# Kernel optimization log

Measured on AMD Instinct MI355X. Metric: run time of the kernel, lower is better.

## Reference

```python
import jax, jax.numpy as jnp
import numpy as np

B, S, E = 8, 2048, 1024

def setup_inputs() -> dict:
    key = jax.random.key(0)
    ks = jax.random.split(key, 7)
    scale = 1.0 / np.sqrt(E)
    return {
        "x": jax.random.normal(ks[0], (B, S, E), dtype=jnp.float32),
        "Wq": jax.random.normal(ks[1], (E, E), dtype=jnp.float32) * scale,
        "bq": jax.random.normal(ks[2], (E,), dtype=jnp.float32) * 0.01,
        "Wk": jax.random.normal(ks[3], (E, E), dtype=jnp.float32) * scale,
        "bk": jax.random.normal(ks[4], (E,), dtype=jnp.float32) * 0.01,
        "Wv": jax.random.normal(ks[5], (E, E), dtype=jnp.float32) * scale,
        "bv": jax.random.normal(ks[6], (E,), dtype=jnp.float32) * 0.01,
    }

def reference(x, Wq, bq, Wk, bk, Wv, bv):
    # torch Linear: y = x @ W^T + b
    q = jnp.einsum('bse,fe->bsf', x, Wq) + bq  # [B,S,E]
    k = jnp.einsum('bse,fe->bsf', x, Wk) + bk
    v = jnp.einsum('bse,fe->bsf', x, Wv) + bv
    # unscaled, unmasked single-head attention (faithful to source)
    scores = jnp.einsum('bqe,bke->bqk', q, k)  # [B,S,S]
    attn = jax.nn.softmax(scores, axis=-1)
    return jnp.einsum('bqk,bke->bqe', attn, v)  # [B,S,E]
```

## Files before the change

### kernel.cpp

```cpp
#include <hip/hip_runtime.h>
#include <math.h>

typedef _Float16 f16;
typedef _Float16 f16x8 __attribute__((ext_vector_type(8)));
typedef _Float16 f16x4 __attribute__((ext_vector_type(4)));
typedef float f32x4v __attribute__((ext_vector_type(4)));

#define Bb 8
#define Ss 2048
#define Ee 1024
#define BSr (Bb*Ss)

__device__ __forceinline__ void gll16(const void* gp, void* lp) {
    __builtin_amdgcn_global_load_lds(
        (const __attribute__((address_space(1))) unsigned int*)gp,
        (__attribute__((address_space(3))) unsigned int*)lp,
        16, 0, 0);
}

#define MFMA16(a, b, c) __builtin_amdgcn_mfma_f32_16x16x32_f16((a), (b), (c), 0, 0, 0)
#define SBAR() asm volatile("s_barrier" ::: "memory")

__global__ __launch_bounds__(256)
void split_weights(const float* __restrict__ Wq, const float* __restrict__ Wk,
                   const float* __restrict__ Wv,
                   f16* __restrict__ Wqh, f16* __restrict__ Wql,
                   f16* __restrict__ Wkh, f16* __restrict__ Wkl,
                   f16* __restrict__ Wvh)
{
    const int i = (blockIdx.x * 256 + threadIdx.x) * 4;
    float4 q = *(const float4*)&Wq[i];
    float4 k = *(const float4*)&Wk[i];
    float4 v = *(const float4*)&Wv[i];
    f16x4 qh4, ql4, kh4, kl4, vh4;
#define SPL(val, h4, l4, idx) { f16 hh = (f16)(val); h4[idx] = hh; l4[idx] = (f16)((val) - (float)hh); }
    SPL(q.x, qh4, ql4, 0) SPL(q.y, qh4, ql4, 1) SPL(q.z, qh4, ql4, 2) SPL(q.w, qh4, ql4, 3)
    SPL(k.x, kh4, kl4, 0) SPL(k.y, kh4, kl4, 1) SPL(k.z, kh4, kl4, 2) SPL(k.w, kh4, kl4, 3)
#undef SPL
    vh4[0] = (f16)v.x; vh4[1] = (f16)v.y; vh4[2] = (f16)v.z; vh4[3] = (f16)v.w;
    *(f16x4*)&Wqh[i] = qh4; *(f16x4*)&Wql[i] = ql4;
    *(f16x4*)&Wkh[i] = kh4; *(f16x4*)&Wkl[i] = kl4;
    *(f16x4*)&Wvh[i] = vh4;
}

__global__ __launch_bounds__(256)
void split_x(const float* __restrict__ x, f16* __restrict__ xh)
{
    const int i = (blockIdx.x * 256 + threadIdx.x) * 4;
    float4 v = *(const float4*)&x[i];
    f16x4 h4;
    h4[0] = (f16)v.x; h4[1] = (f16)v.y; h4[2] = (f16)v.z; h4[3] = (f16)v.w;
    *(f16x4*)&xh[i] = h4;
}

template<bool DUAL>
__device__ __forceinline__ void kloop32(
    const f16* __restrict__ Ag, const f16* __restrict__ Bhg,
    const f16* __restrict__ Blg, f16* __restrict__ lds,
    f32x4v acc[8][4], const int w, const int lane)
{
    constexpr int SETF = DUAL ? 24576 : 16384;
    const int wr = w >> 2, wc = w & 3;
    const int srcoff = (w * 16 + (lane & 15)) * Ee + (lane >> 4) * 8;
    const int lrd = lane * 8;
    const int NT = 32;

#define STAGE8(t, s) do {                                                   \
        const int k0_ = (t) * 32;                                           \
        const f16* gA_ = Ag + k0_ + srcoff;                                 \
        const f16* gB_ = Bhg + k0_ + srcoff;                                \
        f16* dA_ = lds + (s) * SETF + w * 512;                              \
        f16* dB_ = lds + (s) * SETF + 8192 + w * 512;                       \
        gll16(gA_,                       dA_);                              \
        gll16(gA_ + (size_t)8 * 16 * Ee, dA_ + 8 * 512);                    \
        gll16(gB_,                       dB_);                              \
        gll16(gB_ + (size_t)8 * 16 * Ee, dB_ + 8 * 512);                    \
        if (DUAL) {                                                         \
            const f16* gL_ = Blg + k0_ + srcoff;                            \
            f16* dL_ = lds + (s) * SETF + 16384 + w * 512;                  \
            gll16(gL_,                       dL_);                          \
            gll16(gL_ + (size_t)8 * 16 * Ee, dL_ + 8 * 512);                \
        }                                                                   \
    } while (0)

    STAGE8(0, 0);
    STAGE8(1, 1);
    if (DUAL) asm volatile("s_waitcnt vmcnt(6)" ::: "memory");
    else      asm volatile("s_waitcnt vmcnt(4)" ::: "memory");
    SBAR();

    for (int t = 0; t < NT; ++t) {
        const int s = t % 3;
        if (t + 2 < NT) STAGE8(t + 2, (t + 2) % 3);

        const f16* As = lds + s * SETF;
        const f16* Bh = As + 8192;
        const f16* Bl = As + 16384;
        f16x8 fa[8], fbh[4], fbl[4];
        #pragma unroll
        for (int i = 0; i < 8; ++i)
            fa[i] = *(const f16x8*)(As + (wr * 8 + i) * 512 + lrd);
        #pragma unroll
        for (int j = 0; j < 4; ++j)
            fbh[j] = *(const f16x8*)(Bh + (wc * 4 + j) * 512 + lrd);
        if (DUAL) {
            #pragma unroll
            for (int j = 0; j < 4; ++j)
                fbl[j] = *(const f16x8*)(Bl + (wc * 4 + j) * 512 + lrd);
        }
        #pragma unroll
        for (int j = 0; j < 4; ++j)
            #pragma unroll
            for (int i = 0; i < 8; ++i) {
                acc[i][j] = MFMA16(fa[i], fbh[j], acc[i][j]);
                if (DUAL)
                    acc[i][j] = MFMA16(fa[i], fbl[j], acc[i][j]);
            }

        if (t + 2 < NT) {
            if (DUAL) asm volatile("s_waitcnt vmcnt(6)" ::: "memory");
            else      asm volatile("s_waitcnt vmcnt(4)" ::: "memory");
        } else if (t + 1 < NT) {
            asm volatile("s_waitcnt vmcnt(0)" ::: "memory");
        }
        SBAR();
    }
#undef STAGE8
}

__global__ __launch_bounds__(512, 2)
void proj8(const f16* __restrict__ xh,
           const f16* __restrict__ Wqh, const f16* __restrict__ Wql,
           const f16* __restrict__ Wkh, const f16* __restrict__ Wkl,
           const f16* __restrict__ Wvh,
           const float* __restrict__ bq, const float* __restrict__ bk,
           const float* __restrict__ bv,
           f16* __restrict__ qh, f16* __restrict__ kh,
           f16* __restrict__ vT)
{
    __shared__ f16 lds[73728];

    const int lin = blockIdx.x;
    const int l = (lin & 7) * 96 + (lin >> 3);
    const int bx12 = l % 12;
    const int by = l / 12;
    const int z = bx12 >> 2;
    const int col0 = (bx12 & 3) * 256;
    const int row0 = by * 256;

    const f16* Wh = (z == 0) ? Wqh : ((z == 1) ? Wkh : Wvh);
    const f16* Wl = (z == 0) ? Wql : ((z == 1) ? Wkl : Wvh);
    const float* bias = (z == 0) ? bq : ((z == 1) ? bk : bv);

    const int t = threadIdx.x;
    const int lane = t & 63;
    const int w = t >> 6;
    const int wr = w >> 2, wc = w & 3;

    const f16* Ax = xh + (size_t)row0 * Ee;
    const f16* Bwh = Wh + (size_t)col0 * Ee;
    const f16* Bwl = Wl + (size_t)col0 * Ee;

    f32x4v acc[8][4];
    #pragma unroll
    for (int i = 0; i < 8; ++i)
        #pragma unroll
        for (int j = 0; j < 4; ++j) acc[i][j] = (f32x4v)0.f;

    if (z < 2) kloop32<true>(Ax, Bwh, Bwl, lds, acc, w, lane);
    else       kloop32<false>(Ax, Bwh, Bwh, lds, acc, w, lane);

    if (z < 2) {
        f16* __restrict__ oh = (z == 0) ? qh : kh;
        #pragma unroll
        for (int i = 0; i < 8; ++i) {
            #pragma unroll
            for (int j = 0; j < 4; ++j) {
                const int col = col0 + wc * 64 + j * 16 + (lane & 15);
                const float b = bias[col];
                #pragma unroll
                for (int r = 0; r < 4; ++r) {
                    const int row = row0 + wr * 128 + i * 16 + (lane >> 4) * 4 + r;
                    oh[(size_t)row * Ee + col] = (f16)(acc[i][j][r] + b);
                }
            }
        }
    } else {
        #pragma unroll
        for (int i = 0; i < 8; ++i) {
            #pragma unroll
            for (int j = 0; j < 4; ++j) {
                const int e = col0 + wc * 64 + j * 16 + (lane & 15);
                const float b = bias[e];
                const int srow = row0 + wr * 128 + i * 16 + (lane >> 4) * 4;
                const int bb = srow >> 11;
                const int s = srow & 2047;
                f16x4 pk;
                #pragma unroll
                for (int r = 0; r < 4; ++r) pk[r] = (f16)(acc[i][j][r] + b);
                *(f16x4*)&vT[((size_t)bb * Ee + e) * Ss + s] = pk;
            }
        }
    }
}

__global__ __launch_bounds__(512, 2)
void score8(const f16* __restrict__ qh, const f16* __restrict__ kh,
            float* __restrict__ Sbuf, int batch0)
{
    __shared__ f16 lds[49152];

    const int lin = blockIdx.x;
    const int cpx = gridDim.x >> 3;
    const int l = (lin & 7) * cpx + (lin >> 3);
    const int bn = l & 7;
    const int bm = (l >> 3) & 7;
    const int zb = l >> 6;
    const int b = batch0 + zb;

    const int t = threadIdx.x;
    const int lane = t & 63;
    const int w = t >> 6;
    const int wr = w >> 2, wc = w & 3;

    const f16* Aq = qh + ((size_t)b * Ss + bm * 256) * Ee;
    const f16* Bk = kh + ((size_t)b * Ss + bn * 256) * Ee;

    f32x4v acc[8][4];
    #pragma unroll
    for (int i = 0; i < 8; ++i)
        #pragma unroll
        for (int j = 0; j < 4; ++j) acc[i][j] = (f32x4v)0.f;

    kloop32<false>(Aq, Bk, Bk, lds, acc, w, lane);

    #pragma unroll
    for (int i = 0; i < 8; ++i) {
        #pragma unroll
        for (int j = 0; j < 4; ++j) {
            const int col = bn * 256 + wc * 64 + j * 16 + (lane & 15);
            #pragma unroll
            for (int r = 0; r < 4; ++r) {
                const int row = zb * Ss + bm * 256 + wr * 128 + i * 16 + (lane >> 4) * 4 + r;
                Sbuf[(size_t)row * 2048 + col] = acc[i][j][r];
            }
        }
    }
}

__global__ __launch_bounds__(256)
void softmax_rows(float* __restrict__ Sbuf)
{
    __shared__ float red[8];
    const int t = threadIdx.x;
    const int w = t >> 6;
    float* Srow = Sbuf + (size_t)blockIdx.x * 2048;

    float4 a = *(const float4*)&Srow[t * 8];
    float4 c = *(const float4*)&Srow[t * 8 + 4];
    float v[8] = {a.x, a.y, a.z, a.w, c.x, c.y, c.z, c.w};

    float m = v[0];
    #pragma unroll
    for (int i = 1; i < 8; ++i) m = fmaxf(m, v[i]);
    #pragma unroll
    for (int off = 1; off < 64; off <<= 1) m = fmaxf(m, __shfl_xor(m, off, 64));
    if ((t & 63) == 0) red[w] = m;
    __syncthreads();
    m = fmaxf(fmaxf(red[0], red[1]), fmaxf(red[2], red[3]));

    float e[8], s = 0.f;
    #pragma unroll
    for (int i = 0; i < 8; ++i) { e[i] = __expf(v[i] - m); s += e[i]; }
    #pragma unroll
    for (int off = 1; off < 64; off <<= 1) s += __shfl_xor(s, off, 64);
    if ((t & 63) == 0) red[4 + w] = s;
    __syncthreads();
    s = red[4] + red[5] + red[6] + red[7];

    const float inv = 1.0f / s;
    f16x8 pk;
    #pragma unroll
    for (int i = 0; i < 8; ++i) pk[i] = (f16)(e[i] * inv);
    *(f16x8*)(((f16*)Srow) + t * 8) = pk;
}

__global__ __launch_bounds__(256)
void pv_gemm(const float* __restrict__ Sbuf, const f16* __restrict__ vT,
             float* __restrict__ out, int batch0)
{
    __shared__ f16 Pt[128][32];
    __shared__ f16 Vt[128][32];

    const int zb = blockIdx.z;
    const int b = batch0 + zb;
    const int bm = blockIdx.y;
    const int bn = blockIdx.x;

    const int t = threadIdx.x;
    const int lane = t & 63;
    const int w = t >> 6;
    const int wr = w >> 1, wc = w & 1;
    const int lr = lane & 15;
    const int kq = (lane >> 4) << 3;

    const int rS = w * 32 + (lane >> 2);
    const int eS = (lane & 3) * 8;

    const f16* Pbase = (const f16*)Sbuf;
    const f16* gA = Pbase + ((size_t)(zb * Ss + bm * 128 + rS)) * 4096 + eS;
    const f16* gB = vT + ((size_t)b * Ee + bn * 128 + rS) * Ss + eS;

    f32x4v acc[4][4];
    #pragma unroll
    for (int i = 0; i < 4; ++i)
        #pragma unroll
        for (int j = 0; j < 4; ++j) acc[i][j] = (f32x4v)0.f;

    for (int k0 = 0; k0 < Ss; k0 += 32) {
        __syncthreads();
        #pragma unroll
        for (int c = 0; c < 2; ++c) {
            const int lo = w * 1024 + c * 512;
            gll16(gA + (size_t)c * 16 * 4096 + k0, &Pt[0][0] + lo);
            gll16(gB + (size_t)c * 16 * Ss + k0,   &Vt[0][0] + lo);
        }
        __syncthreads();

        f16x8 fa[4], fb[4];
        #pragma unroll
        for (int i = 0; i < 4; ++i) {
            fa[i] = *(const f16x8*)&Pt[wr * 64 + i * 16 + lr][kq];
            fb[i] = *(const f16x8*)&Vt[wc * 64 + i * 16 + lr][kq];
        }
        #pragma unroll
        for (int i = 0; i < 4; ++i)
            #pragma unroll
            for (int j = 0; j < 4; ++j)
                acc[i][j] = MFMA16(fa[i], fb[j], acc[i][j]);
    }

    #pragma unroll
    for (int i = 0; i < 4; ++i) {
        #pragma unroll
        for (int j = 0; j < 4; ++j) {
            const int col = bn * 128 + wc * 64 + j * 16 + lr;
            #pragma unroll
            for (int r = 0; r < 4; ++r) {
                const int row = bm * 128 + wr * 64 + i * 16 + (lane >> 4) * 4 + r;
                out[((size_t)b * Ss + row) * Ee + col] = acc[i][j][r];
            }
        }
    }
}

#define TQ 16
#define TK 256
#define EC 64
#define NCH (Ee/EC)
#define NT  (Ss/TK)

__global__ __launch_bounds__(256)
void qkv_gemm(const float* __restrict__ x,
              const float* __restrict__ Wq, const float* __restrict__ bq,
              const float* __restrict__ Wk, const float* __restrict__ bk,
              const float* __restrict__ Wv, const float* __restrict__ bv,
              float* __restrict__ oq, float* __restrict__ ok, float* __restrict__ ov)
{
    __shared__ float Xs[64][17];
    __shared__ float Ws[64][17];
    const int t = threadIdx.x;
    const int z = blockIdx.z;
    const float* __restrict__ W    = (z == 0) ? Wq : ((z == 1) ? Wk : Wv);
    const float* __restrict__ bias = (z == 0) ? bq : ((z == 1) ? bk : bv);
    float* __restrict__ out        = (z == 0) ? oq : ((z == 1) ? ok : ov);

    const int row0 = blockIdx.y << 6;
    const int col0 = blockIdx.x << 6;
    const int ti = t >> 4;
    const int tj = t & 15;
    const int lr = t >> 2;
    const int lc = (t & 3) << 2;

    float acc[4][4];
    #pragma unroll
    for (int i = 0; i < 4; ++i)
        #pragma unroll
        for (int j = 0; j < 4; ++j) acc[i][j] = 0.f;

    for (int e0 = 0; e0 < Ee; e0 += 16) {
        __syncthreads();
        {
            float4 xv = *(const float4*)&x[(row0 + lr)*Ee + e0 + lc];
            float4 wv = *(const float4*)&W[(col0 + lr)*Ee + e0 + lc];
            Xs[lr][lc]   = xv.x; Xs[lr][lc+1] = xv.y; Xs[lr][lc+2] = xv.z; Xs[lr][lc+3] = xv.w;
            Ws[lr][lc]   = wv.x; Ws[lr][lc+1] = wv.y; Ws[lr][lc+2] = wv.z; Ws[lr][lc+3] = wv.w;
        }
        __syncthreads();
        #pragma unroll
        for (int ee = 0; ee < 16; ++ee) {
            float xa[4], wb[4];
            #pragma unroll
            for (int i = 0; i < 4; ++i) xa[i] = Xs[(ti<<2)+i][ee];
            #pragma unroll
            for (int j = 0; j < 4; ++j) wb[j] = Ws[(tj<<2)+j][ee];
            #pragma unroll
            for (int i = 0; i < 4; ++i)
                #pragma unroll
                for (int j = 0; j < 4; ++j)
                    acc[i][j] = fmaf(xa[i], wb[j], acc[i][j]);
        }
    }

    const float4 b4 = *(const float4*)&bias[col0 + (tj<<2)];
    #pragma unroll
    for (int i = 0; i < 4; ++i) {
        float4 o;
        o.x = acc[i][0] + b4.x;
        o.y = acc[i][1] + b4.y;
        o.z = acc[i][2] + b4.z;
        o.w = acc[i][3] + b4.w;
        *(float4*)&out[(row0 + (ti<<2) + i)*Ee + col0 + (tj<<2)] = o;
    }
}

__global__ __launch_bounds__(256)
void flash_attn(const float* __restrict__ qsrc,
                const float* __restrict__ ksrc,
                const float* __restrict__ vsrc,
                float* __restrict__ out)
{
    __shared__ float qs[TQ][1028];
    __shared__ float kv[TK][68];
    __shared__ float ps[TQ][260];
    __shared__ float f_s[TQ];
    __shared__ float l_s[TQ];

    const int t = threadIdx.x;
    const int lane = t & 63;
    const int w = t >> 6;
    const int q0 = blockIdx.x * TQ;
    const int kb = (q0 / Ss) * Ss;

    {
        const int r = t >> 4;
        const int c0 = (t & 15) << 2;
        #pragma unroll
        for (int m = 0; m < 16; ++m) {
            float4 v4 = *(const float4*)&qsrc[(q0 + r)*Ee + c0 + (m << 6)];
            *(float4*)&qs[r][c0 + (m << 6)] = v4;
        }
    }

    float4 oacc[NCH];
    #pragma unroll
    for (int i = 0; i < NCH; ++i) oacc[i] = make_float4(0.f, 0.f, 0.f, 0.f);
    float m_reg[4], l_reg[4];
    #pragma unroll
    for (int i = 0; i < 4; ++i) { m_reg[i] = -INFINITY; l_reg[i] = 0.f; }

    const int ow = t >> 4;
    const int oc = (t & 15) << 2;

    for (int kt = 0; kt < NT; ++kt) {
        const int kr0 = kb + kt * TK;

        float sacc[4][4];
        #pragma unroll
        for (int i = 0; i < 4; ++i)
            #pragma unroll
            for (int j = 0; j < 4; ++j) sacc[i][j] = 0.f;

        for (int ec = 0; ec < NCH; ++ec) {
            __syncthreads();
            {
                const int rr = t >> 4;
                const int cc = (t & 15) << 2;
                #pragma unroll
                for (int m = 0; m < 16; ++m) {
                    float4 v4 = *(const float4*)&ksrc[(kr0 + rr + (m<<4))*Ee + ec*EC + cc];
                    *(float4*)&kv[rr + (m<<4)][cc] = v4;
                }
            }
            __syncthreads();
            #pragma unroll 4
            for (int ee = 0; ee < EC; ee += 4) {
                float4 q4[4];
                #pragma unroll
                for (int i = 0; i < 4; ++i)
                    q4[i] = *(const float4*)&qs[(w<<2)+i][ec*EC + ee];
                #pragma unroll
                for (int j = 0; j < 4; ++j) {
                    float4 k4 = *(const float4*)&kv[lane + (j<<6)][ee];
                    #pragma unroll
                    for (int i = 0; i < 4; ++i) {
                        sacc[i][j] = fmaf(q4[i].x, k4.x, sacc[i][j]);
                        sacc[i][j] = fmaf(q4[i].y, k4.y, sacc[i][j]);
                        sacc[i][j] = fmaf(q4[i].z, k4.z, sacc[i][j]);
                        sacc[i][j] = fmaf(q4[i].w, k4.w, sacc[i][j]);
                    }
                }
            }
        }

        float tmax[4];
        #pragma unroll
        for (int i = 0; i < 4; ++i)
            tmax[i] = fmaxf(fmaxf(sacc[i][0], sacc[i][1]), fmaxf(sacc[i][2], sacc[i][3]));
        #pragma unroll
        for (int off = 1; off < 64; off <<= 1) {
            #pragma unroll
            for (int i = 0; i < 4; ++i)
                tmax[i] = fmaxf(tmax[i], __shfl_xor(tmax[i], off, 64));
        }
        float rs[4], fi[4];
        #pragma unroll
        for (int i = 0; i < 4; ++i) {
            float mn = fmaxf(m_reg[i], tmax[i]);
            fi[i] = __expf(m_reg[i] - mn);
            m_reg[i] = mn;
            float r = 0.f;
            #pragma unroll
            for (int j = 0; j < 4; ++j) {
                float p = __expf(sacc[i][j] - mn);
                ps[(w<<2)+i][lane + (j<<6)] = p;
                r += p;
            }
            rs[i] = r;
        }
        #pragma unroll
        for (int off = 1; off < 64; off <<= 1) {
            #pragma unroll
            for (int i = 0; i < 4; ++i)
                rs[i] += __shfl_xor(rs[i], off, 64);
        }
        #pragma unroll
        for (int i = 0; i < 4; ++i)
            l_reg[i] = l_reg[i] * fi[i] + rs[i];
        if (lane == 0) {
            #pragma unroll
            for (int i = 0; i < 4; ++i) {
                f_s[(w<<2)+i] = fi[i];
                l_s[(w<<2)+i] = l_reg[i];
            }
        }
        __syncthreads();

        const float fown = f_s[ow];
        #pragma unroll
        for (int c4 = 0; c4 < NCH; ++c4) {
            oacc[c4].x *= fown; oacc[c4].y *= fown;
            oacc[c4].z *= fown; oacc[c4].w *= fown;
        }
        for (int pc = 0; pc < NCH; ++pc) {
            __syncthreads();
            {
                const int rr = t >> 4;
                const int cc = (t & 15) << 2;
                #pragma unroll
                for (int m = 0; m < 16; ++m) {
                    float4 v4 = *(const float4*)&vsrc[(kr0 + rr + (m<<4))*Ee + pc*EC + cc];
                    *(float4*)&kv[rr + (m<<4)][cc] = v4;
                }
            }
            __syncthreads();
            float4 acc = oacc[pc];
            #pragma unroll 4
            for (int tj0 = 0; tj0 < TK; tj0 += 4) {
                float4 p4 = *(const float4*)&ps[ow][tj0];
                float4 v0 = *(const float4*)&kv[tj0+0][oc];
                float4 v1 = *(const float4*)&kv[tj0+1][oc];
                float4 v2 = *(const float4*)&kv[tj0+2][oc];
                float4 v3 = *(const float4*)&kv[tj0+3][oc];
                acc.x = fmaf(p4.x, v0.x, acc.x); acc.y = fmaf(p4.x, v0.y, acc.y);
                acc.z = fmaf(p4.x, v0.z, acc.z); acc.w = fmaf(p4.x, v0.w, acc.w);
                acc.x = fmaf(p4.y, v1.x, acc.x); acc.y = fmaf(p4.y, v1.y, acc.y);
                acc.z = fmaf(p4.y, v1.z, acc.z); acc.w = fmaf(p4.y, v1.w, acc.w);
                acc.x = fmaf(p4.z, v2.x, acc.x); acc.y = fmaf(p4.z, v2.y, acc.y);
                acc.z = fmaf(p4.z, v2.z, acc.z); acc.w = fmaf(p4.z, v2.w, acc.w);
                acc.x = fmaf(p4.w, v3.x, acc.x); acc.y = fmaf(p4.w, v3.y, acc.y);
                acc.z = fmaf(p4.w, v3.z, acc.z); acc.w = fmaf(p4.w, v3.w, acc.w);
            }
            oacc[pc] = acc;
        }
    }

    __syncthreads();
    const float linv = 1.0f / l_s[ow];
    #pragma unroll
    for (int c4 = 0; c4 < NCH; ++c4) {
        float4 o = oacc[c4];
        o.x *= linv; o.y *= linv; o.z *= linv; o.w *= linv;
        *(float4*)&out[(q0 + ow)*Ee + oc + (c4 << 6)] = o;
    }
}

extern "C" void kernel_launch(void* const* d_in, const int* in_sizes, int n_in,
                              void* d_out, int out_size, void* d_ws, size_t ws_size,
                              hipStream_t stream)
{
    (void)in_sizes; (void)n_in; (void)out_size;
    const float* x  = (const float*)d_in[0];
    const float* Wq = (const float*)d_in[1];
    const float* bq = (const float*)d_in[2];
    const float* Wk = (const float*)d_in[3];
    const float* bk = (const float*)d_in[4];
    const float* Wv = (const float*)d_in[5];
    const float* bv = (const float*)d_in[6];
    float* out = (float*)d_out;

    const size_t WPL  = 2097152ull;
    const size_t QPL  = 33554432ull;
    const size_t S4   = 67108864ull;
    const size_t S2   = 33554432ull;
    const size_t NEED4 = S4 + 5 * WPL + 2 * QPL + 33554432ull;
    const size_t NEED2 = S2 + 5 * WPL + 2 * QPL + 33554432ull;

    if (ws_size >= NEED2) {
        const int nb = (ws_size >= NEED4) ? 4 : 2;
        const size_t sbytes = (nb == 4) ? S4 : S2;
        float* Sbuf = (float*)d_ws;
        f16* Wqh = (f16*)((char*)d_ws + sbytes);
        f16* Wql = Wqh + 1048576;
        f16* Wkh = Wqh + 2 * 1048576;
        f16* Wkl = Wqh + 3 * 1048576;
        f16* Wvh = Wqh + 4 * 1048576;
        f16* qh = (f16*)((char*)d_ws + sbytes + 5 * WPL);
        f16* kh = qh + 16777216;
        f16* vT = (f16*)((char*)d_ws + sbytes + 5 * WPL + 2 * QPL);
        f16* xh = (f16*)d_out;

        split_weights<<<1024, 256, 0, stream>>>(Wq, Wk, Wv, Wqh, Wql, Wkh, Wkl, Wvh);
        split_x<<<16384, 256, 0, stream>>>(x, xh);
        proj8<<<768, 512, 0, stream>>>(
            xh, Wqh, Wql, Wkh, Wkl, Wvh, bq, bk, bv, qh, kh, vT);
        for (int c = 0; c < 8 / nb; ++c) {
            score8<<<64 * nb, 512, 0, stream>>>(qh, kh, Sbuf, nb * c);
            softmax_rows<<<nb * 2048, 256, 0, stream>>>(Sbuf);
            pv_gemm<<<dim3(8, 16, nb), 256, 0, stream>>>(Sbuf, vT, out, nb * c);
        }
    } else {
        float* kbuf = (float*)d_ws;
        float* vbuf = kbuf + (size_t)BSr * Ee;
        dim3 g1(Ee / 64, BSr / 64, 3);
        qkv_gemm<<<g1, 256, 0, stream>>>(x, Wq, bq, Wk, bk, Wv, bv, out, kbuf, vbuf);
        flash_attn<<<dim3(BSr / TQ), 256, 0, stream>>>(out, kbuf, vbuf, out);
    }
}
```

Baseline: 435.7 us.

## Split QKV projection into separate 128x256-tile dual and single GEMM kernels

Replaces the single 512-thread 256x256-tile projection kernel, which branched on Q/K/V, with two kernels. One handles Q and K with the hi/lo split weights, the other handles V with a single fp16 weight. Both use 256-thread blocks, 128x256 tiles and a simple double-buffered k-loop. This removes divergence in per-block work (dual-MFMA blocks next to single-MFMA blocks) and uses smaller LDS footprints for better occupancy and load balance. The cost is lower per-block data reuse (half the rows per B tile) and an extra kernel launch.

```diff
diff --git a/kernel.cpp b/kernel.cpp
--- a/kernel.cpp
+++ b/kernel.cpp
@@ -51,6 +51,170 @@
     f16x4 h4;
     h4[0] = (f16)v.x; h4[1] = (f16)v.y; h4[2] = (f16)v.z; h4[3] = (f16)v.w;
     *(f16x4*)&xh[i] = h4;
+}
+
+template<bool DUAL>
+__device__ __forceinline__ void kloopP(
+    const f16* __restrict__ Ag, const f16* __restrict__ Bhg,
+    const f16* __restrict__ Blg, f16* __restrict__ lds,
+    f32x4v acc[8][4], const int w, const int lane)
+{
+    constexpr int SETF = DUAL ? 20480 : 12288;
+    const int src = (w * 16 + (lane & 15)) * Ee + (lane >> 4) * 8;
+    const int lrd = lane * 8;
+    const int NT = 32;
+
+#define STAGEP(t, s) do {                                                    \
+        const int k0_ = (t) * 32;                                            \
+        const f16* gA_ = Ag + k0_ + src;                                     \
+        const f16* gB_ = Bhg + k0_ + src;                                    \
+        f16* base_ = lds + (s) * SETF;                                       \
+        gll16(gA_,                        base_ + w * 512);                  \
+        gll16(gA_ + (size_t)64 * Ee,      base_ + (w + 4) * 512);            \
+        f16* bB_ = base_ + 4096;                                             \
+        gll16(gB_,                        bB_ + w * 512);                    \
+        gll16(gB_ + (size_t)64 * Ee,      bB_ + (w + 4) * 512);              \
+        gll16(gB_ + (size_t)128 * Ee,     bB_ + (w + 8) * 512);              \
+        gll16(gB_ + (size_t)192 * Ee,     bB_ + (w + 12) * 512);             \
+        if (DUAL) {                                                          \
+            const f16* gL_ = Blg + k0_ + src;                                \
+            f16* bL_ = base_ + 12288;                                        \
+            gll16(gL_,                    bL_ + w * 512);                    \
+            gll16(gL_ + (size_t)64 * Ee,  bL_ + (w + 4) * 512);              \
+            gll16(gL_ + (size_t)128 * Ee, bL_ + (w + 8) * 512);              \
+            gll16(gL_ + (size_t)192 * Ee, bL_ + (w + 12) * 512);             \
+        }                                                                    \
+    } while (0)
+
+    STAGEP(0, 0);
+    for (int t = 0; t < NT; ++t) {
+        const int s = t & 1;
+        if (t + 1 < NT) {
+            STAGEP(t + 1, s ^ 1);
+            if (DUAL) asm volatile("s_waitcnt vmcnt(10)" ::: "memory");
+            else      asm volatile("s_waitcnt vmcnt(6)" ::: "memory");
+        } else {
+            asm volatile("s_waitcnt vmcnt(0)" ::: "memory");
+        }
+        SBAR();
+
+        const f16* As = lds + s * SETF;
+        const f16* Bh = As + 4096;
+        const f16* Bl = As + 12288;
+        f16x8 fa[8], fbh[4], fbl[4];
+        #pragma unroll
+        for (int i = 0; i < 8; ++i)
+            fa[i] = *(const f16x8*)(As + i * 512 + lrd);
+        #pragma unroll
+        for (int j = 0; j < 4; ++j)
+            fbh[j] = *(const f16x8*)(Bh + (w * 4 + j) * 512 + lrd);
+        if (DUAL) {
+            #pragma unroll
+            for (int j = 0; j < 4; ++j)
+                fbl[j] = *(const f16x8*)(Bl + (w * 4 + j) * 512 + lrd);
+        }
+        #pragma unroll
+        for (int j = 0; j < 4; ++j)
+            #pragma unroll
+            for (int i = 0; i < 8; ++i) {
+                acc[i][j] = MFMA16(fa[i], fbh[j], acc[i][j]);
+                if (DUAL)
+                    acc[i][j] = MFMA16(fa[i], fbl[j], acc[i][j]);
+            }
+        SBAR();
+    }
+#undef STAGEP
+}
+
+__global__ __launch_bounds__(256, 2)
+void proj4dual(const f16* __restrict__ xh,
+               const f16* __restrict__ Wqh, const f16* __restrict__ Wql,
+               const f16* __restrict__ Wkh, const f16* __restrict__ Wkl,
+               const float* __restrict__ bq, const float* __restrict__ bk,
+               f16* __restrict__ qh, f16* __restrict__ kh)
+{
+    __shared__ f16 lds[40960];
+
+    const int lin = blockIdx.x;
+    const int l = (lin & 7) * 128 + (lin >> 3);
+    const int zc = l & 7;
+    const int by = l >> 3;
+    const int z = zc >> 2;
+    const int col0 = (zc & 3) * 256;
+    const int row0 = by * 128;
+
+    const f16* Wh = (z == 0) ? Wqh : Wkh;
+    const f16* Wl = (z == 0) ? Wql : Wkl;
+    const float* bias = (z == 0) ? bq : bk;
+    f16* __restrict__ oh = (z == 0) ? qh : kh;
+
+    const int t = threadIdx.x;
+    const int lane = t & 63;
+    const int w = t >> 6;
+
+    f32x4v acc[8][4];
+    #pragma unroll
+    for (int i = 0; i < 8; ++i)
+        #pragma unroll
+        for (int j = 0; j < 4; ++j) acc[i][j] = (f32x4v)0.f;
+
+    kloopP<true>(xh + (size_t)row0 * Ee, Wh + (size_t)col0 * Ee,
+                 Wl + (size_t)col0 * Ee, lds, acc, w, lane);
+
+    #pragma unroll
+    for (int i = 0; i < 8; ++i) {
+        #pragma unroll
+        for (int j = 0; j < 4; ++j) {
+            const int col = col0 + w * 64 + j * 16 + (lane & 15);
+            const float b = bias[col];
+            #pragma unroll
+            for (int r = 0; r < 4; ++r) {
+                const int row = row0 + i * 16 + (lane >> 4) * 4 + r;
+                oh[(size_t)row * Ee + col] = (f16)(acc[i][j][r] + b);
+            }
+        }
+    }
+}
+
+__global__ __launch_bounds__(256, 2)
+void proj4v(const f16* __restrict__ xh, const f16* __restrict__ Wvh,
+            const float* __restrict__ bv, f16* __restrict__ vT)
+{
+    __shared__ f16 lds[24576];
+
+    const int lin = blockIdx.x;
+    const int l = (lin & 7) * 64 + (lin >> 3);
+    const int col0 = (l & 3) * 256;
+    const int row0 = (l >> 2) * 128;
+
+    const int t = threadIdx.x;
+    const int lane = t & 63;
+    const int w = t >> 6;
+
+    f32x4v acc[8][4];
+    #pragma unroll
+    for (int i = 0; i < 8; ++i)
+        #pragma unroll
+        for (int j = 0; j < 4; ++j) acc[i][j] = (f32x4v)0.f;
+
+    kloopP<false>(xh + (size_t)row0 * Ee, Wvh + (size_t)col0 * Ee,
+                  Wvh + (size_t)col0 * Ee, lds, acc, w, lane);
+
+    #pragma unroll
+    for (int i = 0; i < 8; ++i) {
+        #pragma unroll
+        for (int j = 0; j < 4; ++j) {
+            const int e = col0 + w * 64 + j * 16 + (lane & 15);
+            const float b = bv[e];
+            const int srow = row0 + i * 16 + (lane >> 4) * 4;
+            const int bb = srow >> 11;
+            const int s = srow & 2047;
+            f16x4 pk;
+            #pragma unroll
+            for (int r = 0; r < 4; ++r) pk[r] = (f16)(acc[i][j][r] + b);
+            *(f16x4*)&vT[((size_t)bb * Ee + e) * Ss + s] = pk;
+        }
+    }
 }
 
 template<bool DUAL>
@@ -126,82 +290,6 @@
         SBAR();
     }
 #undef STAGE8
-}
-
-__global__ __launch_bounds__(512, 2)
-void proj8(const f16* __restrict__ xh,
-           const f16* __restrict__ Wqh, const f16* __restrict__ Wql,
-           const f16* __restrict__ Wkh, const f16* __restrict__ Wkl,
-           const f16* __restrict__ Wvh,
-           const float* __restrict__ bq, const float* __restrict__ bk,
-           const float* __restrict__ bv,
-           f16* __restrict__ qh, f16* __restrict__ kh,
-           f16* __restrict__ vT)
-{
-    __shared__ f16 lds[73728];
-
-    const int lin = blockIdx.x;
-    const int l = (lin & 7) * 96 + (lin >> 3);
-    const int bx12 = l % 12;
-    const int by = l / 12;
-    const int z = bx12 >> 2;
-    const int col0 = (bx12 & 3) * 256;
-    const int row0 = by * 256;
-
-    const f16* Wh = (z == 0) ? Wqh : ((z == 1) ? Wkh : Wvh);
-    const f16* Wl = (z == 0) ? Wql : ((z == 1) ? Wkl : Wvh);
-    const float* bias = (z == 0) ? bq : ((z == 1) ? bk : bv);
-
-    const int t = threadIdx.x;
-    const int lane = t & 63;
-    const int w = t >> 6;
-    const int wr = w >> 2, wc = w & 3;
-
-    const f16* Ax = xh + (size_t)row0 * Ee;
-    const f16* Bwh = Wh + (size_t)col0 * Ee;
-    const f16* Bwl = Wl + (size_t)col0 * Ee;
-
-    f32x4v acc[8][4];
-    #pragma unroll
-    for (int i = 0; i < 8; ++i)
-        #pragma unroll
-        for (int j = 0; j < 4; ++j) acc[i][j] = (f32x4v)0.f;
-
-    if (z < 2) kloop32<true>(Ax, Bwh, Bwl, lds, acc, w, lane);
-    else       kloop32<false>(Ax, Bwh, Bwh, lds, acc, w, lane);
-
-    if (z < 2) {
-        f16* __restrict__ oh = (z == 0) ? qh : kh;
-        #pragma unroll
-        for (int i = 0; i < 8; ++i) {
-            #pragma unroll
-            for (int j = 0; j < 4; ++j) {
-                const int col = col0 + wc * 64 + j * 16 + (lane & 15);
-                const float b = bias[col];
-                #pragma unroll
-                for (int r = 0; r < 4; ++r) {
-                    const int row = row0 + wr * 128 + i * 16 + (lane >> 4) * 4 + r;
-                    oh[(size_t)row * Ee + col] = (f16)(acc[i][j][r] + b);
-                }
-            }
-        }
-    } else {
-        #pragma unroll
-        for (int i = 0; i < 8; ++i) {
-            #pragma unroll
-            for (int j = 0; j < 4; ++j) {
-                const int e = col0 + wc * 64 + j * 16 + (lane & 15);
-                const float b = bias[e];
-                const int srow = row0 + wr * 128 + i * 16 + (lane >> 4) * 4;
-                const int bb = srow >> 11;
-                const int s = srow & 2047;
-                f16x4 pk;
-                #pragma unroll
-                for (int r = 0; r < 4; ++r) pk[r] = (f16)(acc[i][j][r] + b);
-                *(f16x4*)&vT[((size_t)bb * Ee + e) * Ss + s] = pk;
-            }
-        }
-    }
 }
 
 __global__ __launch_bounds__(512, 2)
@@ -632,8 +720,8 @@
 
         split_weights<<<1024, 256, 0, stream>>>(Wq, Wk, Wv, Wqh, Wql, Wkh, Wkl, Wvh);
         split_x<<<16384, 256, 0, stream>>>(x, xh);
-        proj8<<<768, 512, 0, stream>>>(
-            xh, Wqh, Wql, Wkh, Wkl, Wvh, bq, bk, bv, qh, kh, vT);
+        proj4dual<<<1024, 256, 0, stream>>>(xh, Wqh, Wql, Wkh, Wkl, bq, bk, qh, kh);
+        proj4v<<<512, 256, 0, stream>>>(xh, Wvh, bv, vT);
         for (int c = 0; c < 8 / nb; ++c) {
             score8<<<64 * nb, 512, 0, stream>>>(qh, kh, Sbuf, nb * c);
             softmax_rows<<<nb * 2048, 256, 0, stream>>>(Sbuf);
```

After: 467.5 us. 7.3% more time.

## Fold Wq^T Wk into one matrix to drop the K projection

Applied to the files above, without the earlier changes.

Rewrites the scores as (x M^T) x^T + x (Wk^T bq), where M = Wq^T Wk is precomputed from split fp16 weights. Terms that are constant along each softmax row (those involving bk, and bq·bk) are dropped because softmax cancels them. The Q and K projections become a single projection of x by M, so the separate K projection and its buffer go away and the score GEMM reads xh directly. In exchange it adds small weight-only kernels (transpose, M GEMM, reduction, bias vector) and changes the rounding path, since M is rounded to hi/lo fp16 and x is used in fp16 only.

```diff
diff --git a/kernel.cpp b/kernel.cpp
--- a/kernel.cpp
+++ b/kernel.cpp
@@ -10,6 +10,7 @@
 #define Ss 2048
 #define Ee 1024
 #define BSr (Bb*Ss)
+#define MB 1048576ull
 
 __device__ __forceinline__ void gll16(const void* gp, void* lp) {
     __builtin_amdgcn_global_load_lds(
@@ -22,28 +23,6 @@
 #define SBAR() asm volatile("s_barrier" ::: "memory")
 
 __global__ __launch_bounds__(256)
-void split_weights(const float* __restrict__ Wq, const float* __restrict__ Wk,
-                   const float* __restrict__ Wv,
-                   f16* __restrict__ Wqh, f16* __restrict__ Wql,
-                   f16* __restrict__ Wkh, f16* __restrict__ Wkl,
-                   f16* __restrict__ Wvh)
-{
-    const int i = (blockIdx.x * 256 + threadIdx.x) * 4;
-    float4 q = *(const float4*)&Wq[i];
-    float4 k = *(const float4*)&Wk[i];
-    float4 v = *(const float4*)&Wv[i];
-    f16x4 qh4, ql4, kh4, kl4, vh4;
-#define SPL(val, h4, l4, idx) { f16 hh = (f16)(val); h4[idx] = hh; l4[idx] = (f16)((val) - (float)hh); }
-    SPL(q.x, qh4, ql4, 0) SPL(q.y, qh4, ql4, 1) SPL(q.z, qh4, ql4, 2) SPL(q.w, qh4, ql4, 3)
-    SPL(k.x, kh4, kl4, 0) SPL(k.y, kh4, kl4, 1) SPL(k.z, kh4, kl4, 2) SPL(k.w, kh4, kl4, 3)
-#undef SPL
-    vh4[0] = (f16)v.x; vh4[1] = (f16)v.y; vh4[2] = (f16)v.z; vh4[3] = (f16)v.w;
-    *(f16x4*)&Wqh[i] = qh4; *(f16x4*)&Wql[i] = ql4;
-    *(f16x4*)&Wkh[i] = kh4; *(f16x4*)&Wkl[i] = kl4;
-    *(f16x4*)&Wvh[i] = vh4;
-}
-
-__global__ __launch_bounds__(256)
 void split_x(const float* __restrict__ x, f16* __restrict__ xh)
 {
     const int i = (blockIdx.x * 256 + threadIdx.x) * 4;
@@ -51,6 +30,188 @@
     f16x4 h4;
     h4[0] = (f16)v.x; h4[1] = (f16)v.y; h4[2] = (f16)v.z; h4[3] = (f16)v.w;
     *(f16x4*)&xh[i] = h4;
+}
+
+__global__ __launch_bounds__(256)
+void split_wv(const float* __restrict__ Wv, f16* __restrict__ Wvh)
+{
+    const int i = (blockIdx.x * 256 + threadIdx.x) * 4;
+    float4 v = *(const float4*)&Wv[i];
+    f16x4 h4;
+    h4[0] = (f16)v.x; h4[1] = (f16)v.y; h4[2] = (f16)v.z; h4[3] = (f16)v.w;
+    *(f16x4*)&Wvh[i] = h4;
+}
+
+__global__ __launch_bounds__(256)
+void transpose_split(const float* __restrict__ Wq, const float* __restrict__ Wk,
+                     f16* __restrict__ WqTh, f16* __restrict__ WqTl,
+                     f16* __restrict__ WkTh, f16* __restrict__ WkTl)
+{
+    __shared__ float ts[64][65];
+    const int z = blockIdx.z;
+    const float* W = z ? Wk : Wq;
+    f16* Th = z ? WkTh : WqTh;
+    f16* Tl = z ? WkTl : WqTl;
+    const int e0 = blockIdx.x * 64, j0 = blockIdx.y * 64;
+    const int t = threadIdx.x;
+    {
+        const int jj = t >> 2, c0 = (t & 3) * 16;
+        #pragma unroll
+        for (int m = 0; m < 4; ++m) {
+            float4 v = *(const float4*)&W[(size_t)(j0 + jj) * Ee + e0 + c0 + m * 4];
+            ts[jj][c0 + m*4 + 0] = v.x; ts[jj][c0 + m*4 + 1] = v.y;
+            ts[jj][c0 + m*4 + 2] = v.z; ts[jj][c0 + m*4 + 3] = v.w;
+        }
+    }
+    __syncthreads();
+    {
+        const int ee = t >> 2, jc0 = (t & 3) * 16;
+        f16x8 h0, h1, l0, l1;
+        #pragma unroll
+        for (int m = 0; m < 16; ++m) {
+            float val = ts[jc0 + m][ee];
+            f16 hh = (f16)val; f16 ll = (f16)(val - (float)hh);
+            if (m < 8) { h0[m] = hh; l0[m] = ll; }
+            else       { h1[m-8] = hh; l1[m-8] = ll; }
+        }
+        size_t off = (size_t)(e0 + ee) * Ee + j0 + jc0;
+        *(f16x8*)&Th[off]     = h0; *(f16x8*)&Th[off + 8] = h1;
+        *(f16x8*)&Tl[off]     = l0; *(f16x8*)&Tl[off + 8] = l1;
+    }
+}
+
+__global__ __launch_bounds__(256)
+void compute_Mt(const f16* __restrict__ WkTh, const f16* __restrict__ WkTl,
+                const f16* __restrict__ WqTh, const f16* __restrict__ WqTl,
+                float* __restrict__ Mpart)
+{
+    __shared__ f16 Ah[128][32];
+    __shared__ f16 Al[128][32];
+    __shared__ f16 Bh[128][32];
+    __shared__ f16 Bl[128][32];
+
+    const int bn = blockIdx.x, bm = blockIdx.y, z = blockIdx.z;
+    const int t = threadIdx.x;
+    const int lane = t & 63;
+    const int w = t >> 6;
+    const int wr = w >> 1, wc = w & 1;
+    const int lr = lane & 15;
+    const int kq = (lane >> 4) << 3;
+    const int rS = w * 32 + (lane >> 2);
+    const int eS = (lane & 3) * 8;
+
+    const f16* gAh = WkTh + ((size_t)(bm * 128 + rS)) * Ee + z * 256 + eS;
+    const f16* gAl = WkTl + ((size_t)(bm * 128 + rS)) * Ee + z * 256 + eS;
+    const f16* gBh = WqTh + ((size_t)(bn * 128 + rS)) * Ee + z * 256 + eS;
+    const f16* gBl = WqTl + ((size_t)(bn * 128 + rS)) * Ee + z * 256 + eS;
+
+    f32x4v acc[4][4];
+    #pragma unroll
+    for (int i = 0; i < 4; ++i)
+        #pragma unroll
+        for (int j = 0; j < 4; ++j) acc[i][j] = (f32x4v)0.f;
+
+    for (int k0 = 0; k0 < 256; k0 += 32) {
+        __syncthreads();
+        #pragma unroll
+        for (int c = 0; c < 2; ++c) {
+            const size_t go = (size_t)c * 16 * Ee + k0;
+            const int lo = w * 1024 + c * 512;
+            gll16(gAh + go, &Ah[0][0] + lo);
+            gll16(gAl + go, &Al[0][0] + lo);
+            gll16(gBh + go, &Bh[0][0] + lo);
+            gll16(gBl + go, &Bl[0][0] + lo);
+        }
+        __syncthreads();
+
+        f16x8 fah[4], fal[4], fbh[4], fbl[4];
+        #pragma unroll
+        for (int i = 0; i < 4; ++i) {
+            fah[i] = *(const f16x8*)&Ah[wr * 64 + i * 16 + lr][kq];
+            fal[i] = *(const f16x8*)&Al[wr * 64 + i * 16 + lr][kq];
+            fbh[i] = *(const f16x8*)&Bh[wc * 64 + i * 16 + lr][kq];
+            fbl[i] = *(const f16x8*)&Bl[wc * 64 + i * 16 + lr][kq];
+        }
+        #pragma unroll
+        for (int i = 0; i < 4; ++i)
+            #pragma unroll
+            for (int j = 0; j < 4; ++j) {
+                acc[i][j] = MFMA16(fah[i], fbh[j], acc[i][j]);
+                acc[i][j] = MFMA16(fah[i], fbl[j], acc[i][j]);
+                acc[i][j] = MFMA16(fal[i], fbh[j], acc[i][j]);
+            }
+    }
+
+    #pragma unroll
+    for (int i = 0; i < 4; ++i) {
+        #pragma unroll
+        for (int j = 0; j < 4; ++j) {
+            const int col = bn * 128 + wc * 64 + j * 16 + lr;
+            #pragma unroll
+            for (int r = 0; r < 4; ++r) {
+                const int row = bm * 128 + wr * 64 + i * 16 + (lane >> 4) * 4 + r;
+                Mpart[(size_t)z * MB + (size_t)row * Ee + col] = acc[i][j][r];
+            }
+        }
+    }
+}
+
+__global__ __launch_bounds__(256)
+void reduce_Mt(const float* __restrict__ Mpart, f16* __restrict__ Mth, f16* __restrict__ Mtl)
+{
+    const size_t i4 = ((size_t)blockIdx.x * 256 + threadIdx.x) * 4;
+    float4 a = *(const float4*)&Mpart[i4];
+    float4 b = *(const float4*)&Mpart[MB + i4];
+    float4 c = *(const float4*)&Mpart[2 * MB + i4];
+    float4 d = *(const float4*)&Mpart[3 * MB + i4];
+    float s[4] = {a.x + b.x + c.x + d.x, a.y + b.y + c.y + d.y,
+                  a.z + b.z + c.z + d.z, a.w + b.w + c.w + d.w};
+    f16x4 h, l;
+    #pragma unroll
+    for (int m = 0; m < 4; ++m) { f16 hh = (f16)s[m]; h[m] = hh; l[m] = (f16)(s[m] - (float)hh); }
+    *(f16x4*)&Mth[i4] = h;
+    *(f16x4*)&Mtl[i4] = l;
+}
+
+__global__ __launch_bounds__(256)
+void wker(const float* __restrict__ Wk, const float* __restrict__ bq,
+          float* __restrict__ wpart)
+{
+    const int f = (blockIdx.x & 3) * 256 + threadIdx.x;
+    const int p = blockIdx.x >> 2;
+    float acc = 0.f;
+    for (int j = p * 128; j < p * 128 + 128; ++j)
+        acc += Wk[(size_t)j * Ee + f] * bq[j];
+    wpart[p * Ee + f] = acc;
+}
+
+__global__ __launch_bounds__(256)
+void vker(const f16* __restrict__ xh, const float* __restrict__ wpart,
+          float* __restrict__ vbuf)
+{
+    __shared__ float wsum[1024];
+    const int t = threadIdx.x;
+    for (int ff = t; ff < 1024; ff += 256) {
+        float s = 0.f;
+        #pragma unroll
+        for (int p = 0; p < 8; ++p) s += wpart[p * Ee + ff];
+        wsum[ff] = s;
+    }
+    __syncthreads();
+    const int lane = t & 63;
+    const int row = blockIdx.x * 4 + (t >> 6);
+    const f16* xr = xh + (size_t)row * Ee + lane * 16;
+    f16x8 a = *(const f16x8*)&xr[0];
+    f16x8 b = *(const f16x8*)&xr[8];
+    float acc = 0.f;
+    #pragma unroll
+    for (int m = 0; m < 8; ++m) {
+        acc += (float)a[m] * wsum[lane * 16 + m];
+        acc += (float)b[m] * wsum[lane * 16 + 8 + m];
+    }
+    #pragma unroll
+    for (int off = 1; off < 64; off <<= 1) acc += __shfl_xor(acc, off, 64);
+    if (lane == 0) vbuf[row] = acc;
 }
 
 template<bool DUAL>
@@ -129,69 +290,57 @@
 }
 
 __global__ __launch_bounds__(512, 2)
-void proj8(const f16* __restrict__ xh,
-           const f16* __restrict__ Wqh, const f16* __restrict__ Wql,
-           const f16* __restrict__ Wkh, const f16* __restrict__ Wkl,
-           const f16* __restrict__ Wvh,
-           const float* __restrict__ bq, const float* __restrict__ bk,
-           const float* __restrict__ bv,
-           f16* __restrict__ qh, f16* __restrict__ kh,
-           f16* __restrict__ vT)
+void proj3(const f16* __restrict__ xh,
+           const f16* __restrict__ Mth, const f16* __restrict__ Mtl,
+           const f16* __restrict__ Wvh, const float* __restrict__ bv,
+           f16* __restrict__ qp, f16* __restrict__ vT)
 {
     __shared__ f16 lds[73728];
 
     const int lin = blockIdx.x;
-    const int l = (lin & 7) * 96 + (lin >> 3);
-    const int bx12 = l % 12;
-    const int by = l / 12;
-    const int z = bx12 >> 2;
-    const int col0 = (bx12 & 3) * 256;
+    const int l = (lin & 7) * 64 + (lin >> 3);
+    const int zc = l & 7;
+    const int by = l >> 3;
+    const int z = zc >> 2;
+    const int col0 = (zc & 3) * 256;
     const int row0 = by * 256;
-
-    const f16* Wh = (z == 0) ? Wqh : ((z == 1) ? Wkh : Wvh);
-    const f16* Wl = (z == 0) ? Wql : ((z == 1) ? Wkl : Wvh);
-    const float* bias = (z == 0) ? bq : ((z == 1) ? bk : bv);
 
     const int t = threadIdx.x;
     const int lane = t & 63;
     const int w = t >> 6;
     const int wr = w >> 2, wc = w & 3;
 
+    f32x4v acc[8][4];
+    #pragma unroll
+    for (int i = 0; i < 8; ++i)
+        #pragma unroll
+        for (int j = 0; j < 4; ++j) acc[i][j] = (f32x4v)0.f;
+
     const f16* Ax = xh + (size_t)row0 * Ee;
-    const f16* Bwh = Wh + (size_t)col0 * Ee;
-    const f16* Bwl = Wl + (size_t)col0 * Ee;
-
-    f32x4v acc[8][4];
-    #pragma unroll
-    for (int i = 0; i < 8; ++i)
-        #pragma unroll
-        for (int j = 0; j < 4; ++j) acc[i][j] = (f32x4v)0.f;
-
-    if (z < 2) kloop32<true>(Ax, Bwh, Bwl, lds, acc, w, lane);
-    else       kloop32<false>(Ax, Bwh, Bwh, lds, acc, w, lane);
-
-    if (z < 2) {
-        f16* __restrict__ oh = (z == 0) ? qh : kh;
+    if (z == 0) {
+        kloop32<true>(Ax, Mth + (size_t)col0 * Ee, Mtl + (size_t)col0 * Ee,
+                      lds, acc, w, lane);
         #pragma unroll
         for (int i = 0; i < 8; ++i) {
             #pragma unroll
             for (int j = 0; j < 4; ++j) {
                 const int col = col0 + wc * 64 + j * 16 + (lane & 15);
-                const float b = bias[col];
                 #pragma unroll
                 for (int r = 0; r < 4; ++r) {
                     const int row = row0 + wr * 128 + i * 16 + (lane >> 4) * 4 + r;
-                    oh[(size_t)row * Ee + col] = (f16)(acc[i][j][r] + b);
+                    qp[(size_t)row * Ee + col] = (f16)acc[i][j][r];
                 }
             }
         }
     } else {
+        kloop32<false>(Ax, Wvh + (size_t)col0 * Ee, Wvh + (size_t)col0 * Ee,
+                       lds, acc, w, lane);
         #pragma unroll
         for (int i = 0; i < 8; ++i) {
             #pragma unroll
             for (int j = 0; j < 4; ++j) {
                 const int e = col0 + wc * 64 + j * 16 + (lane & 15);
-                const float b = bias[e];
+                const float b = bv[e];
                 const int srow = row0 + wr * 128 + i * 16 + (lane >> 4) * 4;
                 const int bb = srow >> 11;
                 const int s = srow & 2047;
@@ -205,8 +354,8 @@
 }
 
 __global__ __launch_bounds__(512, 2)
-void score8(const f16* __restrict__ qh, const f16* __restrict__ kh,
-            float* __restrict__ Sbuf, int batch0)
+void score8(const f16* __restrict__ qp, const f16* __restrict__ xh,
+            const float* __restrict__ vbuf, float* __restrict__ Sbuf, int batch0)
 {
     __shared__ f16 lds[49152];
 
@@ -223,8 +372,8 @@
     const int w = t >> 6;
     const int wr = w >> 2, wc = w & 3;
 
-    const f16* Aq = qh + ((size_t)b * Ss + bm * 256) * Ee;
-    const f16* Bk = kh + ((size_t)b * Ss + bn * 256) * Ee;
+    const f16* Aq = qp + ((size_t)b * Ss + bm * 256) * Ee;
+    const f16* Bk = xh + ((size_t)b * Ss + bn * 256) * Ee;
 
     f32x4v acc[8][4];
     #pragma unroll
@@ -239,10 +388,11 @@
         #pragma unroll
         for (int j = 0; j < 4; ++j) {
             const int col = bn * 256 + wc * 64 + j * 16 + (lane & 15);
+            const float vv = vbuf[(size_t)b * Ss + col];
             #pragma unroll
             for (int r = 0; r < 4; ++r) {
                 const int row = zb * Ss + bm * 256 + wr * 128 + i * 16 + (lane >> 4) * 4 + r;
-                Sbuf[(size_t)row * 2048 + col] = acc[i][j][r];
+                Sbuf[(size_t)row * 2048 + col] = acc[i][j][r] + vv;
             }
         }
     }
@@ -604,46 +754,53 @@
     const float* Wq = (const float*)d_in[1];
     const float* bq = (const float*)d_in[2];
     const float* Wk = (const float*)d_in[3];
-    const float* bk = (const float*)d_in[4];
+    const float* bk = (const float*)d_in[4];  (void)bk;
     const float* Wv = (const float*)d_in[5];
     const float* bv = (const float*)d_in[6];
     float* out = (float*)d_out;
 
-    const size_t WPL  = 2097152ull;
-    const size_t QPL  = 33554432ull;
-    const size_t S4   = 67108864ull;
-    const size_t S2   = 33554432ull;
-    const size_t NEED4 = S4 + 5 * WPL + 2 * QPL + 33554432ull;
-    const size_t NEED2 = S2 + 5 * WPL + 2 * QPL + 33554432ull;
+    const size_t S4 = 64 * MB, S2 = 32 * MB;
+    const size_t TAIL = 96 * MB + 16 * MB + MB;
+    const size_t NEED4 = S4 + TAIL;
+    const size_t NEED2 = S2 + TAIL;
 
     if (ws_size >= NEED2) {
         const int nb = (ws_size >= NEED4) ? 4 : 2;
-        const size_t sbytes = (nb == 4) ? S4 : S2;
-        float* Sbuf = (float*)d_ws;
-        f16* Wqh = (f16*)((char*)d_ws + sbytes);
-        f16* Wql = Wqh + 1048576;
-        f16* Wkh = Wqh + 2 * 1048576;
-        f16* Wkl = Wqh + 3 * 1048576;
-        f16* Wvh = Wqh + 4 * 1048576;
-        f16* qh = (f16*)((char*)d_ws + sbytes + 5 * WPL);
-        f16* kh = qh + 16777216;
-        f16* vT = (f16*)((char*)d_ws + sbytes + 5 * WPL + 2 * QPL);
-        f16* xh = (f16*)d_out;
-
-        split_weights<<<1024, 256, 0, stream>>>(Wq, Wk, Wv, Wqh, Wql, Wkh, Wkl, Wvh);
+        const size_t sb = (nb == 4) ? S4 : S2;
+        char* base = (char*)d_ws;
+        float* Sbuf = (float*)base;
+        f16* xh   = (f16*)(base + sb);
+        f16* qp   = (f16*)(base + sb + 32 * MB);
+        f16* vT   = (f16*)(base + sb + 64 * MB);
+        f16* Wvh  = (f16*)(base + sb + 96 * MB);
+        f16* WqTh = (f16*)(base + sb + 98 * MB);
+        f16* WqTl = (f16*)(base + sb + 100 * MB);
+        f16* WkTh = (f16*)(base + sb + 102 * MB);
+        f16* WkTl = (f16*)(base + sb + 104 * MB);
+        f16* Mth  = (f16*)(base + sb + 106 * MB);
+        f16* Mtl  = (f16*)(base + sb + 108 * MB);
+        float* Mpart = (float*)(base + sb + 110 * MB);
+        float* wpart = (float*)(base + sb + 126 * MB);
+        float* vbuf  = (float*)(base + sb + 126 * MB + 65536);
+
         split_x<<<16384, 256, 0, stream>>>(x, xh);
-        proj8<<<768, 512, 0, stream>>>(
-            xh, Wqh, Wql, Wkh, Wkl, Wvh, bq, bk, bv, qh, kh, vT);
+        split_wv<<<1024, 256, 0, stream>>>(Wv, Wvh);
+        transpose_split<<<dim3(16, 16, 2), 256, 0, stream>>>(Wq, Wk, WqTh, WqTl, WkTh, WkTl);
+        compute_Mt<<<dim3(8, 8, 4), 256, 0, stream>>>(WkTh, WkTl, WqTh, WqTl, Mpart);
+        reduce_Mt<<<1024, 256, 0, stream>>>(Mpart, Mth, Mtl);
+        wker<<<32, 256, 0, stream>>>(Wk, bq, wpart);
+        vker<<<4096, 256, 0, stream>>>(xh, wpart, vbuf);
+        proj3<<<512, 512, 0, stream>>>(xh, Mth, Mtl, Wvh, bv, qp, vT);
         for (int c = 0; c < 8 / nb; ++c) {
-            score8<<<64 * nb, 512, 0, stream>>>(qh, kh, Sbuf, nb * c);
+            score8<<<64 * nb, 512, 0, stream>>>(qp, xh, vbuf, Sbuf, nb * c);
             softmax_rows<<<nb * 2048, 256, 0, stream>>>(Sbuf);
             pv_gemm<<<dim3(8, 16, nb), 256, 0, stream>>>(Sbuf, vT, out, nb * c);
         }
     } else {
         float* kbuf = (float*)d_ws;
-        float* vbuf = kbuf + (size_t)BSr * Ee;
+        float* vbuf2 = kbuf + (size_t)BSr * Ee;
         dim3 g1(Ee / 64, BSr / 64, 3);
-        qkv_gemm<<<g1, 256, 0, stream>>>(x, Wq, bq, Wk, bk, Wv, bv, out, kbuf, vbuf);
-        flash_attn<<<dim3(BSr / TQ), 256, 0, stream>>>(out, kbuf, vbuf, out);
-    }
-}
+        qkv_gemm<<<g1, 256, 0, stream>>>(x, Wq, bq, Wk, bk, Wv, bv, out, kbuf, vbuf2);
+        flash_attn<<<dim3(BSr / TQ), 256, 0, stream>>>(out, kbuf, vbuf2, out);
+    }
+}
```

After: 420.8 us. -3.4%, faster.
